# Kernel tuning notes

Measured on AMD Instinct MI355X. Metric: run time of the kernel, lower is better.

Reference implementation:

```python
import jax, jax.numpy as jnp
import numpy as np

N, T, U = 8, 200, 50
ENC_DIM = DEC_DIM = JOIN_DIM = 512
VOCAB = 500


def setup_inputs() -> dict:
    key = jax.random.key(0)
    ks = jax.random.split(key, 8)
    s_enc = 1.0 / np.sqrt(ENC_DIM)
    s_dec = 1.0 / np.sqrt(DEC_DIM)
    s_out = 1.0 / np.sqrt(JOIN_DIM)
    return {
        "encoder_out": jax.random.normal(ks[0], (N, T, ENC_DIM), jnp.float32),
        "decoder_out": jax.random.normal(ks[1], (N, U, DEC_DIM), jnp.float32),
        "W_enc": jax.random.normal(ks[2], (JOIN_DIM, ENC_DIM), jnp.float32) * s_enc,
        "b_enc": jax.random.normal(ks[3], (JOIN_DIM,), jnp.float32) * 0.01,
        "W_dec": jax.random.normal(ks[4], (JOIN_DIM, DEC_DIM), jnp.float32) * s_dec,
        "b_dec": jax.random.normal(ks[5], (JOIN_DIM,), jnp.float32) * 0.01,
        "W_out": jax.random.normal(ks[6], (VOCAB, JOIN_DIM), jnp.float32) * s_out,
        "b_out": jax.random.normal(ks[7], (VOCAB,), jnp.float32) * 0.01,
    }


def reference(encoder_out, decoder_out, W_enc, b_enc, W_dec, b_dec, W_out, b_out):
    # Input projections (ScaledLinear == Linear at execution time)
    enc = jnp.einsum("ntc,jc->ntj", encoder_out, W_enc) + b_enc  # (N,T,J)
    dec = jnp.einsum("nuc,jc->nuj", decoder_out, W_dec) + b_dec  # (N,U,J)
    # Broadcast add over (T,U), tanh, then output linear -> (N,T,U,V)
    x = jnp.tanh(enc[:, :, None, :] + dec[:, None, :, :])
    logits = jnp.einsum("ntuj,vj->ntuv", x, W_out) + b_out
    return logits
```

## Files before the change

### kernel.cpp

```cpp
#include <hip/hip_runtime.h>
#include <hip/hip_bf16.h>

typedef __bf16 bf16x8 __attribute__((ext_vector_type(8)));
typedef unsigned short ushort8 __attribute__((ext_vector_type(8)));
typedef unsigned short ushort4v __attribute__((ext_vector_type(4)));
typedef float f32x4 __attribute__((ext_vector_type(4)));

__device__ __forceinline__ unsigned short f2bf(float f) {
    union { float f; unsigned int i; } v;
    v.f = f;
    unsigned int i = v.i;
    i += 0x7fffu + ((i >> 16) & 1u);
    return (unsigned short)(i >> 16);
}

union bfcast { ushort8 u; bf16x8 b; };

__device__ __forceinline__ bf16x8 load_w8_f32(const float* p) {
    const float4 f0 = *(const float4*)p;
    const float4 f1 = *(const float4*)(p + 4);
    bfcast c;
    c.u[0] = f2bf(f0.x); c.u[1] = f2bf(f0.y); c.u[2] = f2bf(f0.z); c.u[3] = f2bf(f0.w);
    c.u[4] = f2bf(f1.x); c.u[5] = f2bf(f1.y); c.u[6] = f2bf(f1.z); c.u[7] = f2bf(f1.w);
    return c.b;
}

__device__ __forceinline__ float fast_tanh(float x) {
    float e = __expf(2.0f * x);
    return 1.0f - 2.0f * __builtin_amdgcn_rcpf(e + 1.0f);
}

__global__ __launch_bounds__(256, 2) void prep_kernel(
    const float* __restrict__ enc_in, const float* __restrict__ dec_in,
    const float* __restrict__ W_enc,  const float* __restrict__ b_enc,
    const float* __restrict__ W_dec,  const float* __restrict__ b_dec,
    const float* __restrict__ W_out,
    float* __restrict__ enc_proj, float* __restrict__ dec_proj,
    unsigned short* __restrict__ wout_bf)
{
    const int blk = blockIdx.x;
    const int tid = threadIdx.x;

    if (blk >= 252) {
        const int e = (blk - 252) * 1024 + tid * 4;
        ushort4v p;
        if (e < 256000) {
            const float4 v = *(const float4*)(W_out + e);
            p.x = f2bf(v.x); p.y = f2bf(v.y); p.z = f2bf(v.z); p.w = f2bf(v.w);
        } else {
            p.x = 0; p.y = 0; p.z = 0; p.w = 0;
        }
        *(ushort4v*)(wout_bf + e) = p;
        return;
    }

    const float *A, *W, *bias; float* outp; int Ma, t, jq;
    if (blk < 200) { A = enc_in; W = W_enc; bias = b_enc; outp = enc_proj;
                     Ma = 1600; t = blk >> 2; jq = blk & 3; }
    else           { const int b2 = blk - 200;
                     A = dec_in; W = W_dec; bias = b_dec; outp = dec_proj;
                     Ma = 400;  t = b2 >> 2;  jq = b2 & 3; }
    const int r0 = t * 32;

    __shared__ unsigned short tile[32 * 520];
    {
        const int row = tid >> 3, q = tid & 7;
        int gr = r0 + row;
        if (gr >= Ma) gr = Ma - 1;
        const float* src = A + (size_t)gr * 512;
        ushort8* dst = (ushort8*)(tile + row * 520);
        #pragma unroll
        for (int i = 0; i < 8; ++i) {
            const int c = q + i * 8;
            const int k = c * 8;
            const float4 a0 = *(const float4*)(src + k);
            const float4 a1 = *(const float4*)(src + k + 4);
            bfcast pk;
            pk.u[0] = f2bf(a0.x); pk.u[1] = f2bf(a0.y); pk.u[2] = f2bf(a0.z); pk.u[3] = f2bf(a0.w);
            pk.u[4] = f2bf(a1.x); pk.u[5] = f2bf(a1.y); pk.u[6] = f2bf(a1.z); pk.u[7] = f2bf(a1.w);
            dst[c] = pk.u;
        }
    }
    __syncthreads();

    const int wave = tid >> 6, lane = tid & 63;
    const int lrow = lane & 15;
    const int lk8  = (lane >> 4) * 8;
    const int j0   = jq * 128 + wave * 32;

    f32x4 acc[2][2];
    #pragma unroll
    for (int mi = 0; mi < 2; ++mi)
        #pragma unroll
        for (int ji = 0; ji < 2; ++ji)
            acc[mi][ji] = (f32x4){0.f, 0.f, 0.f, 0.f};

    const unsigned short* abase = tile + lrow * 520 + lk8;
    const float* wb0 = W + (size_t)(j0 + lrow) * 512 + lk8;
    const float* wb1 = wb0 + 16 * 512;

    #pragma unroll
    for (int kk = 0; kk < 512; kk += 32) {
        const bf16x8 a0 = *(const bf16x8*)(abase + kk);
        const bf16x8 a1 = *(const bf16x8*)(abase + 16 * 520 + kk);
        const bf16x8 b0 = load_w8_f32(wb0 + kk);
        const bf16x8 b1 = load_w8_f32(wb1 + kk);
        acc[0][0] = __builtin_amdgcn_mfma_f32_16x16x32_bf16(a0, b0, acc[0][0], 0, 0, 0);
        acc[0][1] = __builtin_amdgcn_mfma_f32_16x16x32_bf16(a0, b1, acc[0][1], 0, 0, 0);
        acc[1][0] = __builtin_amdgcn_mfma_f32_16x16x32_bf16(a1, b0, acc[1][0], 0, 0, 0);
        acc[1][1] = __builtin_amdgcn_mfma_f32_16x16x32_bf16(a1, b1, acc[1][1], 0, 0, 0);
    }

    const int crow = (lane >> 4) * 4;
    const int ccol = lane & 15;
    #pragma unroll
    for (int ji = 0; ji < 2; ++ji) {
        const int col = j0 + ji * 16 + ccol;
        const float bv = bias[col];
        #pragma unroll
        for (int mi = 0; mi < 2; ++mi)
            #pragma unroll
            for (int rg = 0; rg < 4; ++rg) {
                const int gr = r0 + mi * 16 + crow + rg;
                if (gr < Ma) outp[(size_t)gr * 512 + col] = acc[mi][ji][rg] + bv;
            }
    }
}

__global__ __launch_bounds__(512, 4) void joiner_kernel(
    const float* __restrict__ encp,
    const float* __restrict__ decp,
    const unsigned short* __restrict__ Wout,
    const float* __restrict__ bout,
    float* __restrict__ out)
{
    __shared__ float4 smem[4160];
    unsigned short* tile = (unsigned short*)smem;
    const int tid = threadIdx.x;
    const int r0 = blockIdx.x * 64;

    {
        const int row = tid >> 3, q = tid & 7;
        const int r = r0 + row;
        const int n = r / 10000;
        const int rem = r % 10000;
        const int t = rem / 50;
        const int u = rem - t * 50;
        const float* erow = encp + (size_t)(n * 200 + t) * 512;
        const float* drow = decp + (size_t)(n * 50 + u) * 512;
        ushort8* dst = (ushort8*)(tile + row * 520);
        #pragma unroll
        for (int i = 0; i < 8; ++i) {
            const int c = q + i * 8;
            const int k = c * 8;
            const float4 ev0 = *(const float4*)(erow + k);
            const float4 ev1 = *(const float4*)(erow + k + 4);
            const float4 dv0 = *(const float4*)(drow + k);
            const float4 dv1 = *(const float4*)(drow + k + 4);
            float xs[8] = {ev0.x + dv0.x, ev0.y + dv0.y, ev0.z + dv0.z, ev0.w + dv0.w,
                           ev1.x + dv1.x, ev1.y + dv1.y, ev1.z + dv1.z, ev1.w + dv1.w};
            bfcast pk;
            #pragma unroll
            for (int j = 0; j < 8; ++j) pk.u[j] = f2bf(fast_tanh(xs[j]));
            dst[c] = pk.u;
        }
    }
    __syncthreads();

    const int wave = tid >> 6, lane = tid & 63;
    const int lrow = lane & 15;
    const int lk8  = (lane >> 4) * 8;
    const int v0   = wave * 64;

    f32x4 acc[4][4];
    #pragma unroll
    for (int mi = 0; mi < 4; ++mi)
        #pragma unroll
        for (int ji = 0; ji < 4; ++ji)
            acc[mi][ji] = (f32x4){0.f, 0.f, 0.f, 0.f};

    const unsigned short* wrow[4];
    #pragma unroll
    for (int ji = 0; ji < 4; ++ji)
        wrow[ji] = Wout + (size_t)(v0 + ji * 16 + lrow) * 512 + lk8;
    const unsigned short* abase = tile + lrow * 520 + lk8;

    bf16x8 breg[2][4];
    #pragma unroll
    for (int ji = 0; ji < 4; ++ji) breg[0][ji] = *(const bf16x8*)(wrow[ji]);
    #pragma unroll
    for (int ji = 0; ji < 4; ++ji) breg[1][ji] = *(const bf16x8*)(wrow[ji] + 32);

    #pragma unroll
    for (int kk = 0; kk < 16; ++kk) {
        bf16x8 a[4];
        #pragma unroll
        for (int mi = 0; mi < 4; ++mi)
            a[mi] = *(const bf16x8*)(abase + mi * 16 * 520 + kk * 32);
        bf16x8 bn[4];
        if (kk < 14) {
            #pragma unroll
            for (int ji = 0; ji < 4; ++ji)
                bn[ji] = *(const bf16x8*)(wrow[ji] + (kk + 2) * 32);
        }
        #pragma unroll
        for (int mi = 0; mi < 4; ++mi)
            #pragma unroll
            for (int ji = 0; ji < 4; ++ji)
                acc[mi][ji] = __builtin_amdgcn_mfma_f32_16x16x32_bf16(
                    a[mi], breg[kk & 1][ji], acc[mi][ji], 0, 0, 0);
        if (kk < 14) {
            #pragma unroll
            for (int ji = 0; ji < 4; ++ji) breg[kk & 1][ji] = bn[ji];
        }
    }

    float* ob = (float*)smem;
    const int crow = (lane >> 4) * 4;
    const int ccol = lane & 15;
    const int srow = tid >> 4, sslot = tid & 15;
    #pragma unroll
    for (int h = 0; h < 2; ++h) {
        __syncthreads();
        #pragma unroll
        for (int mi2 = 0; mi2 < 2; ++mi2) {
            const int mi = h * 2 + mi2;
            #pragma unroll
            for (int ji = 0; ji < 4; ++ji) {
                const int v = v0 + ji * 16 + ccol;
                const float bv = (v < 500) ? bout[v] : 0.f;
                #pragma unroll
                for (int rg = 0; rg < 4; ++rg)
                    ob[(mi2 * 16 + crow + rg) * 516 + v] = acc[mi][ji][rg] + bv;
            }
        }
        __syncthreads();
        const size_t gr = (size_t)(r0 + h * 32 + srow);
        const float* src = ob + srow * 516;
        float* drow = out + gr * 500;
        #pragma unroll
        for (int i = 0; i < 8; ++i) {
            const int c = sslot + 16 * i;
            if (c < 125)
                *(float4*)(drow + c * 4) = *(const float4*)(src + c * 4);
        }
    }
}

extern "C" void kernel_launch(void* const* d_in, const int* in_sizes, int n_in,
                              void* d_out, int out_size, void* d_ws, size_t ws_size,
                              hipStream_t stream) {
    (void)in_sizes; (void)n_in; (void)out_size; (void)ws_size;
    const float* enc_in = (const float*)d_in[0];
    const float* dec_in = (const float*)d_in[1];
    const float* W_enc  = (const float*)d_in[2];
    const float* b_enc  = (const float*)d_in[3];
    const float* W_dec  = (const float*)d_in[4];
    const float* b_dec  = (const float*)d_in[5];
    const float* W_out  = (const float*)d_in[6];
    const float* b_out  = (const float*)d_in[7];
    float* out = (float*)d_out;

    float* ws = (float*)d_ws;
    float* enc_proj = ws;
    float* dec_proj = ws + 819200;
    unsigned short* wout_bf = (unsigned short*)(ws + 1024000);

    hipLaunchKernelGGL(prep_kernel, dim3(508), dim3(256), 0, stream,
                       enc_in, dec_in, W_enc, b_enc, W_dec, b_dec, W_out,
                       enc_proj, dec_proj, wout_bf);
    hipLaunchKernelGGL(joiner_kernel, dim3(1250), dim3(512), 0, stream,
                       enc_proj, dec_proj, wout_bf, b_out, out);
}
```

Measured before the change: 262.2 us.

## Halve joiner row tile and use per-wave epilogue with nontemporal stores

Cuts the joiner block tile from 64 to 32 rows and doubles the grid, so each wave keeps 2x4 accumulators instead of 4x4. The output epilogue now stages through a per-wave shared buffer with no block-wide barriers and writes with nontemporal stores. This aims to lower register and LDS pressure, raise occupancy and remove epilogue sync stalls. The cost is that each W_out tile is loaded twice as often across the grid and the output stores become less contiguous.

```diff
diff --git a/kernel.cpp b/kernel.cpp
--- a/kernel.cpp
+++ b/kernel.cpp
@@ -134,13 +134,13 @@
     const float* __restrict__ bout,
     float* __restrict__ out)
 {
-    __shared__ float4 smem[4160];
-    unsigned short* tile = (unsigned short*)smem;
+    __shared__ unsigned short tile[32 * 520];
+    __shared__ float obuf[8][16 * 68];
     const int tid = threadIdx.x;
-    const int r0 = blockIdx.x * 64;
+    const int r0 = blockIdx.x * 32;
 
     {
-        const int row = tid >> 3, q = tid & 7;
+        const int row = tid >> 4, q = tid & 15;
         const int r = r0 + row;
         const int n = r / 10000;
         const int rem = r % 10000;
@@ -150,8 +150,8 @@
         const float* drow = decp + (size_t)(n * 50 + u) * 512;
         ushort8* dst = (ushort8*)(tile + row * 520);
         #pragma unroll
-        for (int i = 0; i < 8; ++i) {
-            const int c = q + i * 8;
+        for (int i = 0; i < 4; ++i) {
+            const int c = q + i * 16;
             const int k = c * 8;
             const float4 ev0 = *(const float4*)(erow + k);
             const float4 ev1 = *(const float4*)(erow + k + 4);
@@ -172,9 +172,9 @@
     const int lk8  = (lane >> 4) * 8;
     const int v0   = wave * 64;
 
-    f32x4 acc[4][4];
-    #pragma unroll
-    for (int mi = 0; mi < 4; ++mi)
+    f32x4 acc[2][4];
+    #pragma unroll
+    for (int mi = 0; mi < 2; ++mi)
         #pragma unroll
         for (int ji = 0; ji < 4; ++ji)
             acc[mi][ji] = (f32x4){0.f, 0.f, 0.f, 0.f};
@@ -193,10 +193,9 @@
 
     #pragma unroll
     for (int kk = 0; kk < 16; ++kk) {
-        bf16x8 a[4];
-        #pragma unroll
-        for (int mi = 0; mi < 4; ++mi)
-            a[mi] = *(const bf16x8*)(abase + mi * 16 * 520 + kk * 32);
+        bf16x8 a[2];
+        a[0] = *(const bf16x8*)(abase + kk * 32);
+        a[1] = *(const bf16x8*)(abase + 16 * 520 + kk * 32);
         bf16x8 bn[4];
         if (kk < 14) {
             #pragma unroll
@@ -204,7 +203,7 @@
                 bn[ji] = *(const bf16x8*)(wrow[ji] + (kk + 2) * 32);
         }
         #pragma unroll
-        for (int mi = 0; mi < 4; ++mi)
+        for (int mi = 0; mi < 2; ++mi)
             #pragma unroll
             for (int ji = 0; ji < 4; ++ji)
                 acc[mi][ji] = __builtin_amdgcn_mfma_f32_16x16x32_bf16(
@@ -215,34 +214,32 @@
         }
     }
 
-    float* ob = (float*)smem;
+    float* ob = obuf[wave];
     const int crow = (lane >> 4) * 4;
     const int ccol = lane & 15;
-    const int srow = tid >> 4, sslot = tid & 15;
-    #pragma unroll
-    for (int h = 0; h < 2; ++h) {
-        __syncthreads();
-        #pragma unroll
-        for (int mi2 = 0; mi2 < 2; ++mi2) {
-            const int mi = h * 2 + mi2;
-            #pragma unroll
-            for (int ji = 0; ji < 4; ++ji) {
-                const int v = v0 + ji * 16 + ccol;
-                const float bv = (v < 500) ? bout[v] : 0.f;
-                #pragma unroll
-                for (int rg = 0; rg < 4; ++rg)
-                    ob[(mi2 * 16 + crow + rg) * 516 + v] = acc[mi][ji][rg] + bv;
+    const int srow = lane >> 2;
+    const int scol = (lane & 3) * 16;
+    #pragma unroll
+    for (int mi = 0; mi < 2; ++mi) {
+        #pragma unroll
+        for (int ji = 0; ji < 4; ++ji) {
+            const int v = v0 + ji * 16 + ccol;
+            const float bv = (v < 500) ? bout[v] : 0.f;
+            #pragma unroll
+            for (int rg = 0; rg < 4; ++rg)
+                ob[(crow + rg) * 68 + ji * 16 + ccol] = acc[mi][ji][rg] + bv;
+        }
+        asm volatile("s_waitcnt lgkmcnt(0)" ::: "memory");
+        const size_t gr = (size_t)(r0 + mi * 16 + srow);
+        float* drow = out + gr * 500;
+        const float* src = ob + srow * 68 + scol;
+        #pragma unroll
+        for (int i = 0; i < 4; ++i) {
+            const int v = v0 + scol + i * 4;
+            if (v < 500) {
+                f32x4 val = *(const f32x4*)(src + i * 4);
+                __builtin_nontemporal_store(val, (f32x4*)(drow + v));
             }
-        }
-        __syncthreads();
-        const size_t gr = (size_t)(r0 + h * 32 + srow);
-        const float* src = ob + srow * 516;
-        float* drow = out + gr * 500;
-        #pragma unroll
-        for (int i = 0; i < 8; ++i) {
-            const int c = sslot + 16 * i;
-            if (c < 125)
-                *(float4*)(drow + c * 4) = *(const float4*)(src + c * 4);
         }
     }
 }
@@ -269,6 +266,6 @@
     hipLaunchKernelGGL(prep_kernel, dim3(508), dim3(256), 0, stream,
                        enc_in, dec_in, W_enc, b_enc, W_dec, b_dec, W_out,
                        enc_proj, dec_proj, wout_bf);
-    hipLaunchKernelGGL(joiner_kernel, dim3(1250), dim3(512), 0, stream,
+    hipLaunchKernelGGL(joiner_kernel, dim3(2500), dim3(512), 0, stream,
                        enc_proj, dec_proj, wout_bf, b_out, out);
 }
```

New measurement: 468.0 us. 78.5% more time.
